# Kernel tuning notes

Hardware: AMD Instinct MI355X
Metric: run time of the kernel (lower is better)

Reference implementation:

```python
import jax, jax.numpy as jnp
import numpy as np

S, B, D, K, E = 2048, 16, 256, 2048, 1048576  # seq_len, batch, input_dim, max_seq_len, n_edges


def setup_inputs() -> dict:
    key = jax.random.key(0)
    k1, k2, k3, k4, k5 = jax.random.split(key, 5)
    M = jax.random.normal(k1, (S, B, D), dtype=jnp.float32)
    W = jax.random.normal(k2, (K, D), dtype=jnp.float32) * (1.0 / np.sqrt(D))
    lengths = jax.random.randint(k3, (B,), 1, S, dtype=jnp.int64)
    edge_batch = jax.random.randint(k4, (E,), 0, B, dtype=jnp.int64)
    edge_ij = jax.random.randint(k5, (E, 2), 0, K, dtype=jnp.int64)
    return {"M": M, "W": W, "lengths": lengths, "edge_batch": edge_batch, "edge_ij": edge_ij}


def reference(M, W, lengths, edge_batch, edge_ij):
    # scale = Linear(input_dim, max_seq_len, bias=False): (S, B, K)
    scale = jnp.einsum('sbd,kd->sbk', M, W)
    # softmax over the sequence dim (dim=0), then permute(1,2,0) -> (B, K, S)
    alpha = jnp.transpose(jax.nn.softmax(scale, axis=0), (1, 2, 0))
    # mask = ones*1e-10 with edges set to 1; mask_copy = zeros with edges set to 1
    mask = jnp.full(alpha.shape, 1e-10, dtype=alpha.dtype)
    mask = mask.at[edge_batch, edge_ij[:, 0], edge_ij[:, 1]].set(1.0)
    mask_copy = jnp.zeros(alpha.shape, dtype=alpha.dtype)
    mask_copy = mask_copy.at[edge_batch, edge_ij[:, 0], edge_ij[:, 1]].set(1.0)
    masked_alpha = alpha * mask
    sums = masked_alpha.sum(-1, keepdims=True)
    scores = (masked_alpha / sums) * mask_copy
    return scores
```

## Files before the change

### kernel.cpp

```cpp
#include <hip/hip_runtime.h>

#define S_LEN 2048
#define B_DIM 16
#define D_DIM 256
#define K_DIM 2048
#define E_NUM 1048576

typedef __attribute__((ext_vector_type(4))) float f32x4;
typedef __attribute__((ext_vector_type(8))) short s16x8;
typedef __attribute__((ext_vector_type(4))) unsigned short u16x4;
typedef __attribute__((ext_vector_type(8))) unsigned short u16x8;

__device__ __forceinline__ unsigned short f2bf(float f) {
    unsigned int u = __float_as_uint(f);
    u += 0x7fffu + ((u >> 16) & 1u);
    return (unsigned short)(u >> 16);
}

__global__ void prep_kernel(const float* __restrict__ W, unsigned short* __restrict__ Wbf,
                            unsigned long long* __restrict__ mw) {
    int bid = blockIdx.x;
    if (bid < 2048) {
        int t = bid * 256 + threadIdx.x;
        ((f32x4*)mw)[t] = (f32x4){0.f, 0.f, 0.f, 0.f};
    } else {
        int t = (bid - 2048) * 256 + threadIdx.x;
        f32x4 v = ((const f32x4*)W)[t];
        u16x4 u;
        u.x = f2bf(v.x); u.y = f2bf(v.y); u.z = f2bf(v.z); u.w = f2bf(v.w);
        ((u16x4*)Wbf)[t] = u;
    }
}

__global__ void maskbuild_kernel(const int* __restrict__ eb, const int* __restrict__ ij,
                                 unsigned long long* __restrict__ mw) {
    int e = blockIdx.x * 256 + threadIdx.x;
    int b = eb[e];
    int i = ij[2 * e];
    int j = ij[2 * e + 1];
    size_t w = ((size_t)(b * K_DIM + i)) * 32 + (j >> 6);
    atomicOr(&mw[w], 1ull << (j & 63));
}

__launch_bounds__(256, 2)
__global__ void gemm_softmax_kernel(const float* __restrict__ M,
                                    const unsigned short* __restrict__ Wbf,
                                    const unsigned long long* __restrict__ mw,
                                    float* __restrict__ out,
                                    float* __restrict__ pm, float* __restrict__ pz,
                                    float* __restrict__ pze) {
    __shared__ unsigned short Msh[64 * 264];
    __shared__ unsigned short Wsh[64 * 264];

    const int tid  = threadIdx.x;
    const int b    = blockIdx.x >> 5;
    const int sblk = blockIdx.x & 31;
    const int s0   = sblk * 64;
    const int lane = tid & 63;
    const int w    = tid >> 6;
    const int r    = lane & 15;
    const int g    = lane >> 4;

    #pragma unroll
    for (int i = 0; i < 16; ++i) {
        int f4  = i * 256 + tid;
        int row = f4 >> 6;
        int c4  = f4 & 63;
        f32x4 v = *(const f32x4*)&M[((size_t)(s0 + row) * B_DIM + b) * D_DIM + c4 * 4];
        u16x4 u;
        u.x = f2bf(v.x); u.y = f2bf(v.y); u.z = f2bf(v.z); u.w = f2bf(v.w);
        *(u16x4*)&Msh[row * 264 + c4 * 4] = u;
    }

    for (int kt = 0; kt < 32; ++kt) {
        __syncthreads();
        const int k0 = kt * 64;
        #pragma unroll
        for (int i = 0; i < 8; ++i) {
            int u8  = i * 256 + tid;
            int row = u8 >> 5;
            int c8  = u8 & 31;
            u16x8 v = *(const u16x8*)&Wbf[(size_t)(k0 + row) * D_DIM + c8 * 8];
            *(u16x8*)&Wsh[row * 264 + c8 * 8] = v;
        }
        __syncthreads();

        f32x4 acc[4];
        #pragma unroll
        for (int st = 0; st < 4; ++st) acc[st] = (f32x4){0.f, 0.f, 0.f, 0.f};

        #pragma unroll
        for (int d = 0; d < 8; ++d) {
            int doff = d * 32 + g * 8;
            s16x8 bf = *(const s16x8*)&Wsh[(w * 16 + r) * 264 + doff];
            #pragma unroll
            for (int st = 0; st < 4; ++st) {
                s16x8 a = *(const s16x8*)&Msh[(st * 16 + r) * 264 + doff];
                acc[st] = __builtin_amdgcn_mfma_f32_16x16x32_bf16(a, bf, acc[st], 0, 0, 0);
            }
        }

        const int kc = k0 + w * 16 + r;
        const unsigned long long w64 = mw[(size_t)(b * K_DIM + kc) * 32 + sblk];

        float mx = acc[0][0];
        #pragma unroll
        for (int st = 0; st < 4; ++st)
            #pragma unroll
            for (int rr = 0; rr < 4; ++rr) mx = fmaxf(mx, acc[st][rr]);
        mx = fmaxf(mx, __shfl_xor(mx, 16));
        mx = fmaxf(mx, __shfl_xor(mx, 32));

        float zs = 0.f, ze = 0.f;
        const size_t obase = (size_t)(b * K_DIM + kc) * S_LEN + s0;
        #pragma unroll
        for (int st = 0; st < 4; ++st) {
            f32x4 ov;
            #pragma unroll
            for (int rr = 0; rr < 4; ++rr) {
                float v = acc[st][rr];
                float e = __expf(v - mx);
                zs += e;
                int pos = st * 16 + g * 4 + rr;
                bool edge = (w64 >> pos) & 1ull;
                ze += edge ? e : 0.f;
                ov[rr] = edge ? v : 0.f;
            }
            *(f32x4*)&out[obase + st * 16 + g * 4] = ov;
        }
        zs += __shfl_xor(zs, 16); zs += __shfl_xor(zs, 32);
        ze += __shfl_xor(ze, 16); ze += __shfl_xor(ze, 32);

        if (lane < 16) {
            size_t pidx = (size_t)(b * 32 + sblk) * K_DIM + kc;
            pm[pidx]  = mx;
            pz[pidx]  = zs;
            pze[pidx] = ze;
        }
    }
}

__global__ void combine_kernel(const float* __restrict__ pm, const float* __restrict__ pz,
                               const float* __restrict__ pze,
                               float* __restrict__ mfin, float* __restrict__ rd) {
    int t = blockIdx.x * 256 + threadIdx.x;
    int b = t >> 11;
    int k = t & 2047;
    float m = -3.4e38f;
    for (int p = 0; p < 32; ++p)
        m = fmaxf(m, pm[(size_t)(b * 32 + p) * K_DIM + k]);
    float Z = 0.f, Ze = 0.f;
    for (int p = 0; p < 32; ++p) {
        size_t idx = (size_t)(b * 32 + p) * K_DIM + k;
        float sc = __expf(pm[idx] - m);
        Z  += pz[idx]  * sc;
        Ze += pze[idx] * sc;
    }
    float denom = 1e-10f * (Z - Ze) + Ze;
    mfin[t] = m;
    rd[t]   = 1.0f / denom;
}

__global__ void edge_score_kernel(const int* __restrict__ eb, const int* __restrict__ ij,
                                  const float* __restrict__ out,
                                  const float* __restrict__ mfin, const float* __restrict__ rd,
                                  float* __restrict__ esc) {
    int e = blockIdx.x * 256 + threadIdx.x;
    int b = eb[e];
    int i = ij[2 * e];
    int j = ij[2 * e + 1];
    int row = b * K_DIM + i;
    float x = out[(size_t)row * S_LEN + j];
    esc[e] = __expf(x - mfin[row]) * rd[row];
}

__global__ void edge_write_kernel(const int* __restrict__ eb, const int* __restrict__ ij,
                                  const float* __restrict__ esc, float* __restrict__ out) {
    int e = blockIdx.x * 256 + threadIdx.x;
    out[(size_t)(eb[e] * K_DIM + ij[2 * e]) * S_LEN + ij[2 * e + 1]] = esc[e];
}

extern "C" void kernel_launch(void* const* d_in, const int* in_sizes, int n_in,
                              void* d_out, int out_size, void* d_ws, size_t ws_size,
                              hipStream_t stream) {
    (void)in_sizes; (void)n_in; (void)ws_size; (void)out_size;
    const float* M  = (const float*)d_in[0];
    const float* W  = (const float*)d_in[1];
    const int* eb   = (const int*)d_in[3];
    const int* ij   = (const int*)d_in[4];
    float* out      = (float*)d_out;
    char* ws        = (char*)d_ws;

    unsigned long long* mw = (unsigned long long*)ws;
    float* pm   = (float*)(ws + 8388608);
    float* pz   = (float*)(ws + 12582912);
    float* pze  = (float*)(ws + 16777216);
    float* mfin = (float*)(ws + 20971520);
    float* rd   = (float*)(ws + 21102592);
    float* esc  = (float*)(ws + 21233664);
    unsigned short* Wbf = (unsigned short*)(ws + 25427968);

    prep_kernel<<<2560, 256, 0, stream>>>(W, Wbf, mw);
    maskbuild_kernel<<<E_NUM / 256, 256, 0, stream>>>(eb, ij, mw);
    gemm_softmax_kernel<<<512, 256, 0, stream>>>(M, Wbf, mw, out, pm, pz, pze);
    combine_kernel<<<128, 256, 0, stream>>>(pm, pz, pze, mfin, rd);
    edge_score_kernel<<<E_NUM / 256, 256, 0, stream>>>(eb, ij, out, mfin, rd, esc);
    edge_write_kernel<<<E_NUM / 256, 256, 0, stream>>>(eb, ij, esc, out);
}
```

Before: 198.6 us.

## Fuse softmax stats and edge scoring into GEMM with online softmax per k-tile

Each block now owns one batch and one 64-row k tile and walks the whole sequence dimension. It keeps an online running max and running sums for the softmax, and prefetches the next M tile into registers while the current tile is being computed. After the sweep, the same block rescores its own edge entries by walking the mask bitmap with ctz. This removes the partial-stat buffers, the combine kernel and both edge gather/scatter kernels. M is converted to bf16 in a batch-major layout inside the prep kernel. In exchange, each block runs a serial 32-step loop with two syncs per step, and the bitmap walk in the epilogue is irregular.

```diff
diff --git a/kernel.cpp b/kernel.cpp
--- a/kernel.cpp
+++ b/kernel.cpp
@@ -17,18 +17,30 @@
     return (unsigned short)(u >> 16);
 }
 
-__global__ void prep_kernel(const float* __restrict__ W, unsigned short* __restrict__ Wbf,
+__global__ void prep_kernel(const float* __restrict__ W, const float* __restrict__ M,
+                            unsigned short* __restrict__ Wbf, unsigned short* __restrict__ Mbf,
                             unsigned long long* __restrict__ mw) {
     int bid = blockIdx.x;
     if (bid < 2048) {
         int t = bid * 256 + threadIdx.x;
         ((f32x4*)mw)[t] = (f32x4){0.f, 0.f, 0.f, 0.f};
-    } else {
+    } else if (bid < 2560) {
         int t = (bid - 2048) * 256 + threadIdx.x;
         f32x4 v = ((const f32x4*)W)[t];
         u16x4 u;
         u.x = f2bf(v.x); u.y = f2bf(v.y); u.z = f2bf(v.z); u.w = f2bf(v.w);
         ((u16x4*)Wbf)[t] = u;
+    } else {
+        int t = (bid - 2560) * 256 + threadIdx.x;
+        f32x4 v = ((const f32x4*)M)[t];
+        int flat4 = t * 4;
+        int d0 = flat4 & 255;
+        int sb = flat4 >> 8;
+        int b  = sb & 15;
+        int s  = sb >> 4;
+        u16x4 u;
+        u.x = f2bf(v.x); u.y = f2bf(v.y); u.z = f2bf(v.z); u.w = f2bf(v.w);
+        *(u16x4*)&Mbf[((size_t)(b * S_LEN + s)) * D_DIM + d0] = u;
     }
 }
 
@@ -43,141 +55,141 @@
 }
 
 __launch_bounds__(256, 2)
-__global__ void gemm_softmax_kernel(const float* __restrict__ M,
-                                    const unsigned short* __restrict__ Wbf,
-                                    const unsigned long long* __restrict__ mw,
-                                    float* __restrict__ out,
-                                    float* __restrict__ pm, float* __restrict__ pz,
-                                    float* __restrict__ pze) {
+__global__ void gemm2_kernel(const unsigned short* __restrict__ Mbf,
+                             const unsigned short* __restrict__ Wbf,
+                             const unsigned long long* __restrict__ mw,
+                             float* __restrict__ out) {
+    __shared__ unsigned short Wsh[64 * 264];
     __shared__ unsigned short Msh[64 * 264];
-    __shared__ unsigned short Wsh[64 * 264];
+    __shared__ float sm_m[64];
+    __shared__ float sm_rd[64];
 
     const int tid  = threadIdx.x;
-    const int b    = blockIdx.x >> 5;
-    const int sblk = blockIdx.x & 31;
-    const int s0   = sblk * 64;
+    const int x    = blockIdx.x;
+    const int b     = ((x & 7) << 1) | ((x >> 3) & 1);
+    const int ktile = x >> 4;
+    const int k0    = ktile * 64;
     const int lane = tid & 63;
     const int w    = tid >> 6;
     const int r    = lane & 15;
     const int g    = lane >> 4;
 
+    const unsigned short* MB = Mbf + (size_t)b * S_LEN * D_DIM;
+
     #pragma unroll
-    for (int i = 0; i < 16; ++i) {
-        int f4  = i * 256 + tid;
-        int row = f4 >> 6;
-        int c4  = f4 & 63;
-        f32x4 v = *(const f32x4*)&M[((size_t)(s0 + row) * B_DIM + b) * D_DIM + c4 * 4];
-        u16x4 u;
-        u.x = f2bf(v.x); u.y = f2bf(v.y); u.z = f2bf(v.z); u.w = f2bf(v.w);
-        *(u16x4*)&Msh[row * 264 + c4 * 4] = u;
-    }
-
-    for (int kt = 0; kt < 32; ++kt) {
-        __syncthreads();
-        const int k0 = kt * 64;
-        #pragma unroll
-        for (int i = 0; i < 8; ++i) {
-            int u8  = i * 256 + tid;
-            int row = u8 >> 5;
-            int c8  = u8 & 31;
-            u16x8 v = *(const u16x8*)&Wbf[(size_t)(k0 + row) * D_DIM + c8 * 8];
-            *(u16x8*)&Wsh[row * 264 + c8 * 8] = v;
-        }
-        __syncthreads();
+    for (int i = 0; i < 8; ++i) {
+        int u8  = i * 256 + tid;
+        int row = u8 >> 5;
+        int c8  = u8 & 31;
+        *(u16x8*)&Wsh[row * 264 + c8 * 8] = *(const u16x8*)&Wbf[(size_t)(k0 + row) * D_DIM + c8 * 8];
+        *(u16x8*)&Msh[row * 264 + c8 * 8] = *(const u16x8*)&MB[(size_t)row * D_DIM + c8 * 8];
+    }
+    __syncthreads();
+
+    const int kc = k0 + w * 16 + r;
+    const size_t orow = (size_t)(b * K_DIM + kc) * S_LEN;
+    const size_t mrow = (size_t)(b * K_DIM + kc) * 32;
+
+    float m_run = -3.4e38f, Z = 0.f, Ze = 0.f;
+    u16x8 mreg[8];
+
+    for (int st_ = 0; st_ < 32; ++st_) {
+        const int s0 = st_ * 64;
+        if (st_ < 31) {
+            #pragma unroll
+            for (int i = 0; i < 8; ++i) {
+                int u8  = i * 256 + tid;
+                int row = u8 >> 5;
+                int c8  = u8 & 31;
+                mreg[i] = *(const u16x8*)&MB[(size_t)(s0 + 64 + row) * D_DIM + c8 * 8];
+            }
+        }
 
         f32x4 acc[4];
         #pragma unroll
-        for (int st = 0; st < 4; ++st) acc[st] = (f32x4){0.f, 0.f, 0.f, 0.f};
+        for (int q = 0; q < 4; ++q) acc[q] = (f32x4){0.f, 0.f, 0.f, 0.f};
 
         #pragma unroll
         for (int d = 0; d < 8; ++d) {
             int doff = d * 32 + g * 8;
             s16x8 bf = *(const s16x8*)&Wsh[(w * 16 + r) * 264 + doff];
             #pragma unroll
-            for (int st = 0; st < 4; ++st) {
-                s16x8 a = *(const s16x8*)&Msh[(st * 16 + r) * 264 + doff];
-                acc[st] = __builtin_amdgcn_mfma_f32_16x16x32_bf16(a, bf, acc[st], 0, 0, 0);
-            }
-        }
-
-        const int kc = k0 + w * 16 + r;
-        const unsigned long long w64 = mw[(size_t)(b * K_DIM + kc) * 32 + sblk];
-
-        float mx = acc[0][0];
-        #pragma unroll
-        for (int st = 0; st < 4; ++st)
-            #pragma unroll
-            for (int rr = 0; rr < 4; ++rr) mx = fmaxf(mx, acc[st][rr]);
-        mx = fmaxf(mx, __shfl_xor(mx, 16));
-        mx = fmaxf(mx, __shfl_xor(mx, 32));
-
+            for (int q = 0; q < 4; ++q) {
+                s16x8 a = *(const s16x8*)&Msh[(q * 16 + r) * 264 + doff];
+                acc[q] = __builtin_amdgcn_mfma_f32_16x16x32_bf16(a, bf, acc[q], 0, 0, 0);
+            }
+        }
+
+        const unsigned long long w64 = mw[mrow + st_];
+
+        float tmx = acc[0][0];
+        #pragma unroll
+        for (int q = 0; q < 4; ++q)
+            #pragma unroll
+            for (int rr = 0; rr < 4; ++rr) tmx = fmaxf(tmx, acc[q][rr]);
+        tmx = fmaxf(tmx, __shfl_xor(tmx, 16));
+        tmx = fmaxf(tmx, __shfl_xor(tmx, 32));
+
+        const float mnew = fmaxf(m_run, tmx);
         float zs = 0.f, ze = 0.f;
-        const size_t obase = (size_t)(b * K_DIM + kc) * S_LEN + s0;
-        #pragma unroll
-        for (int st = 0; st < 4; ++st) {
+        #pragma unroll
+        for (int q = 0; q < 4; ++q) {
             f32x4 ov;
             #pragma unroll
             for (int rr = 0; rr < 4; ++rr) {
-                float v = acc[st][rr];
-                float e = __expf(v - mx);
+                float v = acc[q][rr];
+                float e = __expf(v - mnew);
                 zs += e;
-                int pos = st * 16 + g * 4 + rr;
+                int pos = q * 16 + g * 4 + rr;
                 bool edge = (w64 >> pos) & 1ull;
                 ze += edge ? e : 0.f;
                 ov[rr] = edge ? v : 0.f;
             }
-            *(f32x4*)&out[obase + st * 16 + g * 4] = ov;
+            *(f32x4*)&out[orow + s0 + q * 16 + g * 4] = ov;
         }
         zs += __shfl_xor(zs, 16); zs += __shfl_xor(zs, 32);
         ze += __shfl_xor(ze, 16); ze += __shfl_xor(ze, 32);
 
-        if (lane < 16) {
-            size_t pidx = (size_t)(b * 32 + sblk) * K_DIM + kc;
-            pm[pidx]  = mx;
-            pz[pidx]  = zs;
-            pze[pidx] = ze;
-        }
-    }
-}
-
-__global__ void combine_kernel(const float* __restrict__ pm, const float* __restrict__ pz,
-                               const float* __restrict__ pze,
-                               float* __restrict__ mfin, float* __restrict__ rd) {
-    int t = blockIdx.x * 256 + threadIdx.x;
-    int b = t >> 11;
-    int k = t & 2047;
-    float m = -3.4e38f;
-    for (int p = 0; p < 32; ++p)
-        m = fmaxf(m, pm[(size_t)(b * 32 + p) * K_DIM + k]);
-    float Z = 0.f, Ze = 0.f;
-    for (int p = 0; p < 32; ++p) {
-        size_t idx = (size_t)(b * 32 + p) * K_DIM + k;
-        float sc = __expf(pm[idx] - m);
-        Z  += pz[idx]  * sc;
-        Ze += pze[idx] * sc;
-    }
-    float denom = 1e-10f * (Z - Ze) + Ze;
-    mfin[t] = m;
-    rd[t]   = 1.0f / denom;
-}
-
-__global__ void edge_score_kernel(const int* __restrict__ eb, const int* __restrict__ ij,
-                                  const float* __restrict__ out,
-                                  const float* __restrict__ mfin, const float* __restrict__ rd,
-                                  float* __restrict__ esc) {
-    int e = blockIdx.x * 256 + threadIdx.x;
-    int b = eb[e];
-    int i = ij[2 * e];
-    int j = ij[2 * e + 1];
-    int row = b * K_DIM + i;
-    float x = out[(size_t)row * S_LEN + j];
-    esc[e] = __expf(x - mfin[row]) * rd[row];
-}
-
-__global__ void edge_write_kernel(const int* __restrict__ eb, const int* __restrict__ ij,
-                                  const float* __restrict__ esc, float* __restrict__ out) {
-    int e = blockIdx.x * 256 + threadIdx.x;
-    out[(size_t)(eb[e] * K_DIM + ij[2 * e]) * S_LEN + ij[2 * e + 1]] = esc[e];
+        const float sc = __expf(m_run - mnew);
+        Z  = Z  * sc + zs;
+        Ze = Ze * sc + ze;
+        m_run = mnew;
+
+        __syncthreads();
+        if (st_ < 31) {
+            #pragma unroll
+            for (int i = 0; i < 8; ++i) {
+                int u8  = i * 256 + tid;
+                int row = u8 >> 5;
+                int c8  = u8 & 31;
+                *(u16x8*)&Msh[row * 264 + c8 * 8] = mreg[i];
+            }
+        }
+        __syncthreads();
+    }
+
+    if (g == 0) {
+        sm_m[w * 16 + r]  = m_run;
+        sm_rd[w * 16 + r] = 1.0f / (1e-10f * (Z - Ze) + Ze);
+    }
+    __threadfence();
+    __syncthreads();
+
+    for (int it = tid; it < 64 * 32; it += 256) {
+        const int kl = it >> 5;
+        const int wj = it & 31;
+        unsigned long long bits = mw[(size_t)(b * K_DIM + k0 + kl) * 32 + wj];
+        if (!bits) continue;
+        const size_t rowo = (size_t)(b * K_DIM + k0 + kl) * S_LEN + wj * 64;
+        const float mm = sm_m[kl];
+        const float rdv = sm_rd[kl];
+        while (bits) {
+            const int j = __builtin_ctzll(bits);
+            bits &= bits - 1;
+            const float xv = out[rowo + j];
+            out[rowo + j] = __expf(xv - mm) * rdv;
+        }
+    }
 }
 
 extern "C" void kernel_launch(void* const* d_in, const int* in_sizes, int n_in,
@@ -192,18 +204,10 @@
     char* ws        = (char*)d_ws;
 
     unsigned long long* mw = (unsigned long long*)ws;
-    float* pm   = (float*)(ws + 8388608);
-    float* pz   = (float*)(ws + 12582912);
-    float* pze  = (float*)(ws + 16777216);
-    float* mfin = (float*)(ws + 20971520);
-    float* rd   = (float*)(ws + 21102592);
-    float* esc  = (float*)(ws + 21233664);
-    unsigned short* Wbf = (unsigned short*)(ws + 25427968);
-
-    prep_kernel<<<2560, 256, 0, stream>>>(W, Wbf, mw);
+    unsigned short* Wbf = (unsigned short*)(ws + 8388608);
+    unsigned short* Mbf = (unsigned short*)(ws + 9437184);
+
+    prep_kernel<<<10752, 256, 0, stream>>>(W, M, Wbf, Mbf, mw);
     maskbuild_kernel<<<E_NUM / 256, 256, 0, stream>>>(eb, ij, mw);
-    gemm_softmax_kernel<<<512, 256, 0, stream>>>(M, Wbf, mw, out, pm, pz, pze);
-    combine_kernel<<<128, 256, 0, stream>>>(pm, pz, pze, mfin, rd);
-    edge_score_kernel<<<E_NUM / 256, 256, 0, stream>>>(eb, ij, out, mfin, rd, esc);
-    edge_write_kernel<<<E_NUM / 256, 256, 0, stream>>>(eb, ij, esc, out);
-}
+    gemm2_kernel<<<512, 256, 0, stream>>>(Mbf, Wbf, mw, out);
+}
```

Result: slower. 254.3 us (+28.0%).
